# Kernel optimization log

Measured on AMD Instinct MI355X. Metric: run time of the kernel, lower is better.

## Reference

```python
import jax, jax.numpy as jnp
import numpy as np

N_NODES = 100000
N_EDGES = 800000
H_DIM = 128
E_DIM = 32
N_LAYER = 3


def setup_inputs() -> dict:
    key = jax.random.key(0)
    ks = jax.random.split(key, 5)
    x = jax.random.normal(ks[0], (N_NODES, H_DIM), dtype=jnp.float32)
    edge_index = jax.random.randint(ks[1], (2, N_EDGES), 0, N_NODES, dtype=jnp.int64)
    edge_attr = jax.random.normal(ks[2], (N_EDGES, E_DIM), dtype=jnp.float32)
    fan_in = 2 * H_DIM + E_DIM
    # torch Linear weight layout: [out_features, in_features]
    Wm = jax.random.normal(ks[3], (N_LAYER, H_DIM, fan_in), dtype=jnp.float32) / jnp.sqrt(fan_in)
    bm = jax.random.normal(ks[4], (N_LAYER, H_DIM), dtype=jnp.float32) * 0.01
    return {"x": x, "edge_index": edge_index, "edge_attr": edge_attr, "Wm": Wm, "bm": bm}


def reference(x, edge_index, edge_attr, Wm, bm):
    # PyG flow='source_to_target': row 0 = source (j), row 1 = target (i)
    src = edge_index[0]
    dst = edge_index[1]
    n_nodes = x.shape[0]
    n_layer = Wm.shape[0]
    for l in range(n_layer):  # small fixed layer count
        # message: m_ij = Linear(cat[x_j, x_i, edge_attr])
        m = jnp.concatenate([x[src], x[dst], edge_attr], axis=1)  # [E, 2h+e]
        m = jnp.einsum('ef,hf->eh', m, Wm[l]) + bm[l]             # [E, h]
        # aggr='add': scatter-add messages to target nodes
        x = jax.ops.segment_sum(m, dst, num_segments=n_nodes)     # [N, h]
        x = jax.nn.leaky_relu(x, negative_slope=0.01)
    # residual_connection='none' -> no-op; activate_last=True
    x = jax.nn.leaky_relu(x, negative_slope=0.01)
    return x
```

## Files before the change

kernel.cpp:

```cpp
#include <hip/hip_runtime.h>

#define N_NODES 100000
#define NP      100096
#define N_EDGES 800000
#define HD 128
#define ED 32
#define FAN 288
#define NL 3

#define SCHUNK 2048
#define SBLK   ((N_NODES + SCHUNK - 1) / SCHUNK)

#define TM 32

typedef short bf16x8 __attribute__((ext_vector_type(8)));
typedef short bf16x4 __attribute__((ext_vector_type(4)));
typedef float f32x4  __attribute__((ext_vector_type(4)));

__device__ inline float b2f(short s) {
    unsigned u = ((unsigned)(unsigned short)s) << 16;
    return __builtin_bit_cast(float, u);
}
__device__ inline short f2b(float f) {
    unsigned u = __builtin_bit_cast(unsigned, f);
    unsigned r = u + 0x7FFFu + ((u >> 16) & 1u);
    return (short)(r >> 16);
}


__global__ void count_kernel(const int* __restrict__ dst, int* __restrict__ deg) {
    int e = blockIdx.x * 256 + threadIdx.x;
    if (e < N_EDGES) atomicAdd(&deg[dst[e]], 1);
}

__global__ void scan_reduce(const int* __restrict__ deg, int* __restrict__ bsum) {
    __shared__ int ws[4];
    const int tid = threadIdx.x;
    int i0 = blockIdx.x * SCHUNK + tid * 8;
    int t = 0;
    #pragma unroll
    for (int j = 0; j < 8; ++j) {
        int i = i0 + j;
        if (i < N_NODES) t += deg[i];
    }
    #pragma unroll
    for (int off = 32; off >= 1; off >>= 1) t += __shfl_down(t, off, 64);
    if ((tid & 63) == 0) ws[tid >> 6] = t;
    __syncthreads();
    if (tid == 0) bsum[blockIdx.x] = ws[0] + ws[1] + ws[2] + ws[3];
}

__global__ void scan_final(const int* __restrict__ deg, const int* __restrict__ bsum,
                           int* __restrict__ ptr, int* __restrict__ cursor) {
    __shared__ int wsum[4];
    __shared__ int s_boff;
    const int tid = threadIdx.x;
    const int lane = tid & 63, wid = tid >> 6;
    if (wid == 0) {
        int v = (lane < SBLK) ? bsum[lane] : 0;
        int s = v;
        #pragma unroll
        for (int off = 1; off < 64; off <<= 1) {
            int t = __shfl_up(s, off, 64);
            if (lane >= off) s += t;
        }
        int srcl = (blockIdx.x == 0) ? 0 : (int)blockIdx.x - 1;
        int bprev = __shfl(s, srcl, 64);
        if (lane == 0) s_boff = (blockIdx.x == 0) ? 0 : bprev;
        int total = __shfl(s, SBLK - 1, 64);
        if (blockIdx.x == 0 && lane == 0) ptr[N_NODES] = total;
    }
    __syncthreads();

    int i0 = blockIdx.x * SCHUNK + tid * 8;
    int v[8]; int tsum = 0;
    #pragma unroll
    for (int j = 0; j < 8; ++j) {
        int i = i0 + j;
        v[j] = (i < N_NODES) ? deg[i] : 0;
        tsum += v[j];
    }
    int s = tsum;
    #pragma unroll
    for (int off = 1; off < 64; off <<= 1) {
        int t = __shfl_up(s, off, 64);
        if (lane >= off) s += t;
    }
    if (lane == 63) wsum[wid] = s;
    __syncthreads();
    int woff = 0;
    #pragma unroll
    for (int w = 0; w < 4; ++w) if (w < wid) woff += wsum[w];
    int excl = s_boff + woff + (s - tsum);
    #pragma unroll
    for (int j = 0; j < 8; ++j) {
        int i = i0 + j;
        if (i < N_NODES) { ptr[i] = excl; cursor[i] = excl; }
        excl += v[j];
    }
}

__global__ void fill_kernel(const int* __restrict__ src, const int* __restrict__ dst,
                            int* __restrict__ cursor, int2* __restrict__ csr2) {
    int e = blockIdx.x * 256 + threadIdx.x;
    if (e < N_EDGES) {
        int d = dst[e];
        int slot = atomicAdd(&cursor[d], 1);
        csr2[slot] = make_int2(src[e], e);
    }
}

__global__ void edge_sum(const int2* __restrict__ csr2, const int* __restrict__ ptr,
                         const float* __restrict__ eattr,
                         short* __restrict__ agge, float* __restrict__ degf) {
    int node = blockIdx.x * 32 + (threadIdx.x >> 3);
    int g = threadIdx.x & 7;
    if (node >= N_NODES) return;
    int s0 = ptr[node], s1 = ptr[node + 1];
    float4 a0 = make_float4(0.f,0.f,0.f,0.f), a1 = make_float4(0.f,0.f,0.f,0.f);
    int s = s0;
    int e0 = (s     < s1) ? csr2[s].y     : 0;
    int e1 = (s + 1 < s1) ? csr2[s + 1].y : 0;
    int e2 = (s + 2 < s1) ? csr2[s + 2].y : 0;
    int e3 = (s + 3 < s1) ? csr2[s + 3].y : 0;
    while (s + 4 <= s1) {
        float4 v0 = *reinterpret_cast<const float4*>(eattr + (size_t)e0 * ED + g * 4);
        float4 v1 = *reinterpret_cast<const float4*>(eattr + (size_t)e1 * ED + g * 4);
        float4 v2 = *reinterpret_cast<const float4*>(eattr + (size_t)e2 * ED + g * 4);
        float4 v3 = *reinterpret_cast<const float4*>(eattr + (size_t)e3 * ED + g * 4);
        s += 4;
        e0 = (s     < s1) ? csr2[s].y     : 0;
        e1 = (s + 1 < s1) ? csr2[s + 1].y : 0;
        e2 = (s + 2 < s1) ? csr2[s + 2].y : 0;
        e3 = (s + 3 < s1) ? csr2[s + 3].y : 0;
        a0.x += v0.x; a0.y += v0.y; a0.z += v0.z; a0.w += v0.w;
        a1.x += v1.x; a1.y += v1.y; a1.z += v1.z; a1.w += v1.w;
        a0.x += v2.x; a0.y += v2.y; a0.z += v2.z; a0.w += v2.w;
        a1.x += v3.x; a1.y += v3.y; a1.z += v3.z; a1.w += v3.w;
    }
    int rem = s1 - s;
    if (rem > 0) {
        float4 v = *reinterpret_cast<const float4*>(eattr + (size_t)e0 * ED + g * 4);
        a0.x += v.x; a0.y += v.y; a0.z += v.z; a0.w += v.w;
    }
    if (rem > 1) {
        float4 v = *reinterpret_cast<const float4*>(eattr + (size_t)e1 * ED + g * 4);
        a1.x += v.x; a1.y += v.y; a1.z += v.z; a1.w += v.w;
    }
    if (rem > 2) {
        float4 v = *reinterpret_cast<const float4*>(eattr + (size_t)e2 * ED + g * 4);
        a0.x += v.x; a0.y += v.y; a0.z += v.z; a0.w += v.w;
    }
    bf16x4 o;
    o[0] = f2b(a0.x + a1.x); o[1] = f2b(a0.y + a1.y);
    o[2] = f2b(a0.z + a1.z); o[3] = f2b(a0.w + a1.w);
    *reinterpret_cast<bf16x4*>(agge + (size_t)node * ED + g * 4) = o;
    if (g == 0) degf[node] = (float)(s1 - s0);
}

#define NW4 (NL * HD * FAN / 4)
#define NX4 (N_NODES * (HD / 4))
__global__ void conv_kernel(const float* __restrict__ Wm, short* __restrict__ Wb,
                            const float* __restrict__ x, short* __restrict__ xb) {
    int i4 = blockIdx.x * 256 + threadIdx.x;
    if (i4 < NW4) {
        float4 v = reinterpret_cast<const float4*>(Wm)[i4];
        bf16x4 o;
        o[0] = f2b(v.x); o[1] = f2b(v.y); o[2] = f2b(v.z); o[3] = f2b(v.w);
        reinterpret_cast<bf16x4*>(Wb)[i4] = o;
    }
    int j4 = i4 - NW4;
    if (j4 >= 0 && j4 < NX4) {
        float4 v = reinterpret_cast<const float4*>(x)[j4];
        bf16x4 o;
        o[0] = f2b(v.x); o[1] = f2b(v.y); o[2] = f2b(v.z); o[3] = f2b(v.w);
        reinterpret_cast<bf16x4*>(xb)[j4] = o;
    }
}

__global__ __launch_bounds__(256) void fused_layer(
    const int* __restrict__ ptr, const int2* __restrict__ csr2,
    const short* __restrict__ xprev,
    const short* __restrict__ agge,
    const float* __restrict__ degf,
    const short* __restrict__ Wb,
    const float* __restrict__ b,
    float* __restrict__ out_f32,
    short* __restrict__ out_x,
    int last)
{
    __shared__ char As[TM * 256];
    const int tid = threadIdx.x;
    const int m0 = blockIdx.x * TM;

    {
        const int ng = tid >> 4, g = tid & 15;
        #pragma unroll
        for (int i = 0; i < 2; ++i) {
            int row = i * 16 + ng;
            int node = m0 + row;
            float acc0[8] = {}, acc1[8] = {};
            if (node < N_NODES) {
                int s0 = ptr[node], s1 = ptr[node + 1];
                int s = s0;
                int i0 = (s     < s1) ? csr2[s].x     : 0;
                int i1 = (s + 1 < s1) ? csr2[s + 1].x : 0;
                int i2 = (s + 2 < s1) ? csr2[s + 2].x : 0;
                int i3 = (s + 3 < s1) ? csr2[s + 3].x : 0;
                while (s + 4 <= s1) {
                    bf16x8 v0 = *reinterpret_cast<const bf16x8*>(xprev + (size_t)i0 * HD + g * 8);
                    bf16x8 v1 = *reinterpret_cast<const bf16x8*>(xprev + (size_t)i1 * HD + g * 8);
                    bf16x8 v2 = *reinterpret_cast<const bf16x8*>(xprev + (size_t)i2 * HD + g * 8);
                    bf16x8 v3 = *reinterpret_cast<const bf16x8*>(xprev + (size_t)i3 * HD + g * 8);
                    s += 4;
                    i0 = (s     < s1) ? csr2[s].x     : 0;
                    i1 = (s + 1 < s1) ? csr2[s + 1].x : 0;
                    i2 = (s + 2 < s1) ? csr2[s + 2].x : 0;
                    i3 = (s + 3 < s1) ? csr2[s + 3].x : 0;
                    #pragma unroll
                    for (int j = 0; j < 8; ++j) acc0[j] += b2f(v0[j]);
                    #pragma unroll
                    for (int j = 0; j < 8; ++j) acc1[j] += b2f(v1[j]);
                    #pragma unroll
                    for (int j = 0; j < 8; ++j) acc0[j] += b2f(v2[j]);
                    #pragma unroll
                    for (int j = 0; j < 8; ++j) acc1[j] += b2f(v3[j]);
                }
                int rem = s1 - s;
                if (rem > 0) {
                    bf16x8 v = *reinterpret_cast<const bf16x8*>(xprev + (size_t)i0 * HD + g * 8);
                    #pragma unroll
                    for (int j = 0; j < 8; ++j) acc0[j] += b2f(v[j]);
                }
                if (rem > 1) {
                    bf16x8 v = *reinterpret_cast<const bf16x8*>(xprev + (size_t)i1 * HD + g * 8);
                    #pragma unroll
                    for (int j = 0; j < 8; ++j) acc1[j] += b2f(v[j]);
                }
                if (rem > 2) {
                    bf16x8 v = *reinterpret_cast<const bf16x8*>(xprev + (size_t)i2 * HD + g * 8);
                    #pragma unroll
                    for (int j = 0; j < 8; ++j) acc0[j] += b2f(v[j]);
                }
            }
            bf16x8 o;
            #pragma unroll
            for (int j = 0; j < 8; ++j) o[j] = f2b(acc0[j] + acc1[j]);
            int byte = row * 256 + g * 16;
            byte ^= (row & 7) << 4;
            *reinterpret_cast<bf16x8*>(As + byte) = o;
        }
    }
    __syncthreads();

    const int w = tid >> 6, lane = tid & 63;
    const int l15 = lane & 15, lq = lane >> 4;
    const int kb = lq * 8;

    f32x4 acc1[2][2], acc2[2][2];
    #pragma unroll
    for (int i = 0; i < 2; ++i)
        #pragma unroll
        for (int j = 0; j < 2; ++j) {
            acc1[i][j] = (f32x4){0.f, 0.f, 0.f, 0.f};
            acc2[i][j] = (f32x4){0.f, 0.f, 0.f, 0.f};
        }

    #pragma unroll
    for (int kt = 0; kt < 4; ++kt) {
        bf16x8 a[2], bf[2];
        #pragma unroll
        for (int mf = 0; mf < 2; ++mf) {
            int row = mf * 16 + l15;
            int byte = row * 256 + kt * 64 + kb * 2;
            byte ^= (row & 7) << 4;
            a[mf] = *reinterpret_cast<const bf16x8*>(As + byte);
        }
        #pragma unroll
        for (int nf = 0; nf < 2; ++nf) {
            int c = w * 32 + nf * 16 + l15;
            bf[nf] = *reinterpret_cast<const bf16x8*>(Wb + (size_t)c * FAN + kt * 32 + kb);
        }
        #pragma unroll
        for (int mf = 0; mf < 2; ++mf)
            #pragma unroll
            for (int nf = 0; nf < 2; ++nf)
                acc1[mf][nf] = __builtin_amdgcn_mfma_f32_16x16x32_bf16(
                    a[mf], bf[nf], acc1[mf][nf], 0, 0, 0);
    }
    #pragma unroll
    for (int kt = 4; kt < 9; ++kt) {
        bf16x8 a[2], bf[2];
        #pragma unroll
        for (int mf = 0; mf < 2; ++mf) {
            size_t arow = (size_t)(m0 + mf * 16 + l15);
            a[mf] = (kt < 8)
                ? *reinterpret_cast<const bf16x8*>(xprev + arow * HD + (kt * 32 - 128) + kb)
                : *reinterpret_cast<const bf16x8*>(agge + arow * ED + kb);
        }
        #pragma unroll
        for (int nf = 0; nf < 2; ++nf) {
            int c = w * 32 + nf * 16 + l15;
            bf[nf] = *reinterpret_cast<const bf16x8*>(Wb + (size_t)c * FAN + kt * 32 + kb);
        }
        #pragma unroll
        for (int mf = 0; mf < 2; ++mf)
            #pragma unroll
            for (int nf = 0; nf < 2; ++nf) {
                if (kt < 8)
                    acc2[mf][nf] = __builtin_amdgcn_mfma_f32_16x16x32_bf16(
                        a[mf], bf[nf], acc2[mf][nf], 0, 0, 0);
                else
                    acc1[mf][nf] = __builtin_amdgcn_mfma_f32_16x16x32_bf16(
                        a[mf], bf[nf], acc1[mf][nf], 0, 0, 0);
            }
    }

    #pragma unroll
    for (int mf = 0; mf < 2; ++mf) {
        int r0 = m0 + mf * 16 + lq * 4;
        float dg[4];
        #pragma unroll
        for (int j = 0; j < 4; ++j)
            dg[j] = (r0 + j < N_NODES) ? degf[r0 + j] : 0.f;
        #pragma unroll
        for (int nf = 0; nf < 2; ++nf) {
            int c = w * 32 + nf * 16 + l15;
            float bc = b[c];
            #pragma unroll
            for (int j = 0; j < 4; ++j) {
                int row = r0 + j;
                if (row >= N_NODES) continue;
                float v = acc1[mf][nf][j] + dg[j] * (acc2[mf][nf][j] + bc);
                v = (v >= 0.f) ? v : 0.01f * v;
                if (last) {
                    v = (v >= 0.f) ? v : 0.01f * v;
                    out_f32[(size_t)row * HD + c] = v;
                } else {
                    out_x[(size_t)row * HD + c] = f2b(v);
                }
            }
        }
    }
}

extern "C" void kernel_launch(void* const* d_in, const int* in_sizes, int n_in,
                              void* d_out, int out_size, void* d_ws, size_t ws_size,
                              hipStream_t stream) {
    const float* x_in  = (const float*)d_in[0];
    const int*   ei    = (const int*)d_in[1];
    const float* eattr = (const float*)d_in[2];
    const float* Wm    = (const float*)d_in[3];
    const float* bm    = (const float*)d_in[4];
    float* out = (float*)d_out;

    char* ws = (char*)d_ws;
    size_t off = 0;
    auto alloc = [&](size_t bytes) -> void* {
        void* p = ws + off;
        off = (off + bytes + 255) & ~(size_t)255;
        return p;
    };
    short* x0      = (short*)alloc((size_t)NP * HD * 2);
    short* x1      = (short*)alloc((size_t)NP * HD * 2);
    short* agge    = (short*)alloc((size_t)NP * ED * 2);
    float* degf    = (float*)alloc((size_t)NP * 4);
    int*   deg     = (int*)alloc((size_t)N_NODES * 4);
    int*   ptr     = (int*)alloc((size_t)(N_NODES + 1) * 4);
    int*   cursor  = (int*)alloc((size_t)N_NODES * 4);
    int2*  csr2    = (int2*)alloc((size_t)N_EDGES * 8);
    short* Wb      = (short*)alloc((size_t)NL * HD * FAN * 2);
    int*   bsum    = (int*)alloc((size_t)SBLK * 4);

    const int* src = ei;
    const int* dst = ei + N_EDGES;

    hipMemsetAsync(deg, 0, (size_t)N_NODES * 4, stream);
    count_kernel<<<(N_EDGES + 255) / 256, 256, 0, stream>>>(dst, deg);
    scan_reduce<<<SBLK, 256, 0, stream>>>(deg, bsum);
    scan_final<<<SBLK, 256, 0, stream>>>(deg, bsum, ptr, cursor);
    fill_kernel<<<(N_EDGES + 255) / 256, 256, 0, stream>>>(src, dst, cursor, csr2);
    edge_sum<<<(N_NODES + 31) / 32, 256, 0, stream>>>(csr2, ptr, eattr, agge, degf);
    conv_kernel<<<(NW4 + NX4 + 255) / 256, 256, 0, stream>>>(Wm, Wb, x_in, x0);

    short* xping[2] = {x0, x1};
    for (int l = 0; l < NL; ++l) {
        fused_layer<<<NP / TM, 256, 0, stream>>>(
            ptr, csr2, xping[l & 1], agge, degf,
            Wb + (size_t)l * HD * FAN, bm + (size_t)l * HD,
            out, xping[(l + 1) & 1], (l == NL - 1) ? 1 : 0);
    }
}
```

Measured before the change: 348.4 us.

## Prescale x by degree into a separate buffer and halve the row tile

Adds a second bf16 copy of node features that is pre-multiplied by in-degree. It is produced in conv_kernel and in each layer's epilogue, so the GEMM can accumulate into one set of accumulators instead of two. The fused layer also shrinks to 16 rows and 128 threads per block, with each wave covering 64 output columns. The aim is lower register pressure and higher occupancy. The cost is an extra full feature-array write per layer, more weight reloads per row, and an extra bf16 rounding of deg*x.

```diff
diff --git a/kernel.cpp b/kernel.cpp
--- a/kernel.cpp
+++ b/kernel.cpp
@@ -11,7 +11,8 @@
 #define SCHUNK 2048
 #define SBLK   ((N_NODES + SCHUNK - 1) / SCHUNK)
 
-#define TM 32
+#define TM 16
+#define THREADS 128
 
 typedef short bf16x8 __attribute__((ext_vector_type(8)));
 typedef short bf16x4 __attribute__((ext_vector_type(4)));
@@ -161,7 +162,8 @@
 #define NW4 (NL * HD * FAN / 4)
 #define NX4 (N_NODES * (HD / 4))
 __global__ void conv_kernel(const float* __restrict__ Wm, short* __restrict__ Wb,
-                            const float* __restrict__ x, short* __restrict__ xb) {
+                            const float* __restrict__ x, const float* __restrict__ degf,
+                            short* __restrict__ xb, short* __restrict__ xd) {
     int i4 = blockIdx.x * 256 + threadIdx.x;
     if (i4 < NW4) {
         float4 v = reinterpret_cast<const float4*>(Wm)[i4];
@@ -171,22 +173,33 @@
     }
     int j4 = i4 - NW4;
     if (j4 >= 0 && j4 < NX4) {
+        int row = j4 >> 5;
+        float d = degf[row];
         float4 v = reinterpret_cast<const float4*>(x)[j4];
-        bf16x4 o;
-        o[0] = f2b(v.x); o[1] = f2b(v.y); o[2] = f2b(v.z); o[3] = f2b(v.w);
+        float vv[4] = {v.x, v.y, v.z, v.w};
+        bf16x4 o, od;
+        #pragma unroll
+        for (int j = 0; j < 4; ++j) {
+            short s = f2b(vv[j]);
+            o[j] = s;
+            od[j] = f2b(b2f(s) * d);
+        }
         reinterpret_cast<bf16x4*>(xb)[j4] = o;
-    }
-}
-
-__global__ __launch_bounds__(256) void fused_layer(
+        reinterpret_cast<bf16x4*>(xd)[j4] = od;
+    }
+}
+
+__global__ __launch_bounds__(THREADS) void fused_layer(
     const int* __restrict__ ptr, const int2* __restrict__ csr2,
     const short* __restrict__ xprev,
+    const short* __restrict__ xdeg,
     const short* __restrict__ agge,
     const float* __restrict__ degf,
     const short* __restrict__ Wb,
     const float* __restrict__ b,
     float* __restrict__ out_f32,
     short* __restrict__ out_x,
+    short* __restrict__ out_xd,
     int last)
 {
     __shared__ char As[TM * 256];
@@ -197,7 +210,7 @@
         const int ng = tid >> 4, g = tid & 15;
         #pragma unroll
         for (int i = 0; i < 2; ++i) {
-            int row = i * 16 + ng;
+            int row = i * 8 + ng;
             int node = m0 + row;
             float acc0[8] = {}, acc1[8] = {};
             if (node < N_NODES) {
@@ -257,87 +270,61 @@
     const int l15 = lane & 15, lq = lane >> 4;
     const int kb = lq * 8;
 
-    f32x4 acc1[2][2], acc2[2][2];
-    #pragma unroll
-    for (int i = 0; i < 2; ++i)
-        #pragma unroll
-        for (int j = 0; j < 2; ++j) {
-            acc1[i][j] = (f32x4){0.f, 0.f, 0.f, 0.f};
-            acc2[i][j] = (f32x4){0.f, 0.f, 0.f, 0.f};
-        }
+    f32x4 acc[4];
+    #pragma unroll
+    for (int j = 0; j < 4; ++j) acc[j] = (f32x4){0.f, 0.f, 0.f, 0.f};
 
     #pragma unroll
     for (int kt = 0; kt < 4; ++kt) {
-        bf16x8 a[2], bf[2];
-        #pragma unroll
-        for (int mf = 0; mf < 2; ++mf) {
-            int row = mf * 16 + l15;
-            int byte = row * 256 + kt * 64 + kb * 2;
-            byte ^= (row & 7) << 4;
-            a[mf] = *reinterpret_cast<const bf16x8*>(As + byte);
-        }
-        #pragma unroll
-        for (int nf = 0; nf < 2; ++nf) {
-            int c = w * 32 + nf * 16 + l15;
-            bf[nf] = *reinterpret_cast<const bf16x8*>(Wb + (size_t)c * FAN + kt * 32 + kb);
-        }
-        #pragma unroll
-        for (int mf = 0; mf < 2; ++mf)
-            #pragma unroll
-            for (int nf = 0; nf < 2; ++nf)
-                acc1[mf][nf] = __builtin_amdgcn_mfma_f32_16x16x32_bf16(
-                    a[mf], bf[nf], acc1[mf][nf], 0, 0, 0);
+        int byte = l15 * 256 + kt * 64 + kb * 2;
+        byte ^= (l15 & 7) << 4;
+        bf16x8 a = *reinterpret_cast<const bf16x8*>(As + byte);
+        #pragma unroll
+        for (int nf = 0; nf < 4; ++nf) {
+            int c = w * 64 + nf * 16 + l15;
+            bf16x8 bfr = *reinterpret_cast<const bf16x8*>(Wb + (size_t)c * FAN + kt * 32 + kb);
+            acc[nf] = __builtin_amdgcn_mfma_f32_16x16x32_bf16(a, bfr, acc[nf], 0, 0, 0);
+        }
     }
     #pragma unroll
     for (int kt = 4; kt < 9; ++kt) {
-        bf16x8 a[2], bf[2];
-        #pragma unroll
-        for (int mf = 0; mf < 2; ++mf) {
-            size_t arow = (size_t)(m0 + mf * 16 + l15);
-            a[mf] = (kt < 8)
-                ? *reinterpret_cast<const bf16x8*>(xprev + arow * HD + (kt * 32 - 128) + kb)
-                : *reinterpret_cast<const bf16x8*>(agge + arow * ED + kb);
-        }
-        #pragma unroll
-        for (int nf = 0; nf < 2; ++nf) {
-            int c = w * 32 + nf * 16 + l15;
-            bf[nf] = *reinterpret_cast<const bf16x8*>(Wb + (size_t)c * FAN + kt * 32 + kb);
-        }
-        #pragma unroll
-        for (int mf = 0; mf < 2; ++mf)
-            #pragma unroll
-            for (int nf = 0; nf < 2; ++nf) {
-                if (kt < 8)
-                    acc2[mf][nf] = __builtin_amdgcn_mfma_f32_16x16x32_bf16(
-                        a[mf], bf[nf], acc2[mf][nf], 0, 0, 0);
-                else
-                    acc1[mf][nf] = __builtin_amdgcn_mfma_f32_16x16x32_bf16(
-                        a[mf], bf[nf], acc1[mf][nf], 0, 0, 0);
-            }
-    }
-
-    #pragma unroll
-    for (int mf = 0; mf < 2; ++mf) {
-        int r0 = m0 + mf * 16 + lq * 4;
+        size_t arow = (size_t)(m0 + l15);
+        bf16x8 a = (kt < 8)
+            ? *reinterpret_cast<const bf16x8*>(xdeg + arow * HD + (kt * 32 - 128) + kb)
+            : *reinterpret_cast<const bf16x8*>(agge + arow * ED + kb);
+        #pragma unroll
+        for (int nf = 0; nf < 4; ++nf) {
+            int c = w * 64 + nf * 16 + l15;
+            bf16x8 bfr = *reinterpret_cast<const bf16x8*>(Wb + (size_t)c * FAN + kt * 32 + kb);
+            acc[nf] = __builtin_amdgcn_mfma_f32_16x16x32_bf16(a, bfr, acc[nf], 0, 0, 0);
+        }
+    }
+
+    __syncthreads();
+
+    {
+        int r0 = m0 + lq * 4;
         float dg[4];
         #pragma unroll
         for (int j = 0; j < 4; ++j)
             dg[j] = (r0 + j < N_NODES) ? degf[r0 + j] : 0.f;
         #pragma unroll
-        for (int nf = 0; nf < 2; ++nf) {
-            int c = w * 32 + nf * 16 + l15;
+        for (int nf = 0; nf < 4; ++nf) {
+            int c = w * 64 + nf * 16 + l15;
             float bc = b[c];
             #pragma unroll
             for (int j = 0; j < 4; ++j) {
                 int row = r0 + j;
                 if (row >= N_NODES) continue;
-                float v = acc1[mf][nf][j] + dg[j] * (acc2[mf][nf][j] + bc);
+                float v = acc[nf][j] + dg[j] * bc;
                 v = (v >= 0.f) ? v : 0.01f * v;
                 if (last) {
                     v = (v >= 0.f) ? v : 0.01f * v;
                     out_f32[(size_t)row * HD + c] = v;
                 } else {
-                    out_x[(size_t)row * HD + c] = f2b(v);
+                    short xb = f2b(v);
+                    out_x[(size_t)row * HD + c] = xb;
+                    out_xd[(size_t)row * HD + c] = f2b(b2f(xb) * dg[j]);
                 }
             }
         }
@@ -363,6 +350,7 @@
     };
     short* x0      = (short*)alloc((size_t)NP * HD * 2);
     short* x1      = (short*)alloc((size_t)NP * HD * 2);
+    short* xdeg    = (short*)alloc((size_t)NP * HD * 2);
     short* agge    = (short*)alloc((size_t)NP * ED * 2);
     float* degf    = (float*)alloc((size_t)NP * 4);
     int*   deg     = (int*)alloc((size_t)N_NODES * 4);
@@ -381,13 +369,13 @@
     scan_final<<<SBLK, 256, 0, stream>>>(deg, bsum, ptr, cursor);
     fill_kernel<<<(N_EDGES + 255) / 256, 256, 0, stream>>>(src, dst, cursor, csr2);
     edge_sum<<<(N_NODES + 31) / 32, 256, 0, stream>>>(csr2, ptr, eattr, agge, degf);
-    conv_kernel<<<(NW4 + NX4 + 255) / 256, 256, 0, stream>>>(Wm, Wb, x_in, x0);
+    conv_kernel<<<(NW4 + NX4 + 255) / 256, 256, 0, stream>>>(Wm, Wb, x_in, degf, x0, xdeg);
 
     short* xping[2] = {x0, x1};
     for (int l = 0; l < NL; ++l) {
-        fused_layer<<<NP / TM, 256, 0, stream>>>(
-            ptr, csr2, xping[l & 1], agge, degf,
+        fused_layer<<<NP / TM, THREADS, 0, stream>>>(
+            ptr, csr2, xping[l & 1], xdeg, agge, degf,
             Wb + (size_t)l * HD * FAN, bm + (size_t)l * HD,
-            out, xping[(l + 1) & 1], (l == NL - 1) ? 1 : 0);
-    }
-}
+            out, xping[(l + 1) & 1], xdeg, (l == NL - 1) ? 1 : 0);
+    }
+}
```

After: 353.3 us. Within noise of the previous version (+1.4%).

## Split CSR into SoA arrays with int4 index loads and prescale x by degree

Applied to the files above, without the earlier changes.

The interleaved int2 CSR is split into separate source-index and edge-id arrays. The gather loops in edge_sum and fused_layer now read indices four at a time as aligned int4 vectors, with masking at the segment edges. A degree-scaled bf16 copy of x (xdeg) is also kept and updated each layer. The self-term GEMM then uses it directly, which merges the two MFMA accumulators into one and simplifies the epilogue. In exchange, each layer writes an extra bf16 node-feature array, rounding changes slightly because x·deg is rounded to bf16 before the matmul, and xdeg is updated in place.

```diff
diff --git a/kernel.cpp b/kernel.cpp
--- a/kernel.cpp
+++ b/kernel.cpp
@@ -101,16 +101,18 @@
 }
 
 __global__ void fill_kernel(const int* __restrict__ src, const int* __restrict__ dst,
-                            int* __restrict__ cursor, int2* __restrict__ csr2) {
+                            int* __restrict__ cursor,
+                            int* __restrict__ csr_src, int* __restrict__ csr_eid) {
     int e = blockIdx.x * 256 + threadIdx.x;
     if (e < N_EDGES) {
         int d = dst[e];
         int slot = atomicAdd(&cursor[d], 1);
-        csr2[slot] = make_int2(src[e], e);
-    }
-}
-
-__global__ void edge_sum(const int2* __restrict__ csr2, const int* __restrict__ ptr,
+        csr_src[slot] = src[e];
+        csr_eid[slot] = e;
+    }
+}
+
+__global__ void edge_sum(const int* __restrict__ csr_eid, const int* __restrict__ ptr,
                          const float* __restrict__ eattr,
                          short* __restrict__ agge, float* __restrict__ degf) {
     int node = blockIdx.x * 32 + (threadIdx.x >> 3);
@@ -118,38 +120,41 @@
     if (node >= N_NODES) return;
     int s0 = ptr[node], s1 = ptr[node + 1];
     float4 a0 = make_float4(0.f,0.f,0.f,0.f), a1 = make_float4(0.f,0.f,0.f,0.f);
-    int s = s0;
-    int e0 = (s     < s1) ? csr2[s].y     : 0;
-    int e1 = (s + 1 < s1) ? csr2[s + 1].y : 0;
-    int e2 = (s + 2 < s1) ? csr2[s + 2].y : 0;
-    int e3 = (s + 3 < s1) ? csr2[s + 3].y : 0;
-    while (s + 4 <= s1) {
-        float4 v0 = *reinterpret_cast<const float4*>(eattr + (size_t)e0 * ED + g * 4);
-        float4 v1 = *reinterpret_cast<const float4*>(eattr + (size_t)e1 * ED + g * 4);
-        float4 v2 = *reinterpret_cast<const float4*>(eattr + (size_t)e2 * ED + g * 4);
-        float4 v3 = *reinterpret_cast<const float4*>(eattr + (size_t)e3 * ED + g * 4);
-        s += 4;
-        e0 = (s     < s1) ? csr2[s].y     : 0;
-        e1 = (s + 1 < s1) ? csr2[s + 1].y : 0;
-        e2 = (s + 2 < s1) ? csr2[s + 2].y : 0;
-        e3 = (s + 3 < s1) ? csr2[s + 3].y : 0;
-        a0.x += v0.x; a0.y += v0.y; a0.z += v0.z; a0.w += v0.w;
-        a1.x += v1.x; a1.y += v1.y; a1.z += v1.z; a1.w += v1.w;
-        a0.x += v2.x; a0.y += v2.y; a0.z += v2.z; a0.w += v2.w;
-        a1.x += v3.x; a1.y += v3.y; a1.z += v3.z; a1.w += v3.w;
-    }
-    int rem = s1 - s;
-    if (rem > 0) {
-        float4 v = *reinterpret_cast<const float4*>(eattr + (size_t)e0 * ED + g * 4);
-        a0.x += v.x; a0.y += v.y; a0.z += v.z; a0.w += v.w;
-    }
-    if (rem > 1) {
-        float4 v = *reinterpret_cast<const float4*>(eattr + (size_t)e1 * ED + g * 4);
-        a1.x += v.x; a1.y += v.y; a1.z += v.z; a1.w += v.w;
-    }
-    if (rem > 2) {
-        float4 v = *reinterpret_cast<const float4*>(eattr + (size_t)e2 * ED + g * 4);
-        a0.x += v.x; a0.y += v.y; a0.z += v.z; a0.w += v.w;
+    int b0 = s0 >> 2;
+    int nb = ((s1 + 3) >> 2) - b0;
+    const int4* ep = (const int4*)csr_eid + b0;
+    int4 cur = (nb > 0) ? ep[0] : make_int4(0,0,0,0);
+    for (int t = 0; t < nb; ++t) {
+        int4 nxt = (t + 1 < nb) ? ep[t + 1] : make_int4(0,0,0,0);
+        int base = (b0 + t) * 4;
+        if (base >= s0 && base + 4 <= s1) {
+            float4 v0 = *reinterpret_cast<const float4*>(eattr + (size_t)cur.x * ED + g * 4);
+            float4 v1 = *reinterpret_cast<const float4*>(eattr + (size_t)cur.y * ED + g * 4);
+            float4 v2 = *reinterpret_cast<const float4*>(eattr + (size_t)cur.z * ED + g * 4);
+            float4 v3 = *reinterpret_cast<const float4*>(eattr + (size_t)cur.w * ED + g * 4);
+            a0.x += v0.x; a0.y += v0.y; a0.z += v0.z; a0.w += v0.w;
+            a1.x += v1.x; a1.y += v1.y; a1.z += v1.z; a1.w += v1.w;
+            a0.x += v2.x; a0.y += v2.y; a0.z += v2.z; a0.w += v2.w;
+            a1.x += v3.x; a1.y += v3.y; a1.z += v3.z; a1.w += v3.w;
+        } else {
+            if (base + 0 >= s0 && base + 0 < s1) {
+                float4 v = *reinterpret_cast<const float4*>(eattr + (size_t)cur.x * ED + g * 4);
+                a0.x += v.x; a0.y += v.y; a0.z += v.z; a0.w += v.w;
+            }
+            if (base + 1 >= s0 && base + 1 < s1) {
+                float4 v = *reinterpret_cast<const float4*>(eattr + (size_t)cur.y * ED + g * 4);
+                a1.x += v.x; a1.y += v.y; a1.z += v.z; a1.w += v.w;
+            }
+            if (base + 2 >= s0 && base + 2 < s1) {
+                float4 v = *reinterpret_cast<const float4*>(eattr + (size_t)cur.z * ED + g * 4);
+                a0.x += v.x; a0.y += v.y; a0.z += v.z; a0.w += v.w;
+            }
+            if (base + 3 >= s0 && base + 3 < s1) {
+                float4 v = *reinterpret_cast<const float4*>(eattr + (size_t)cur.w * ED + g * 4);
+                a1.x += v.x; a1.y += v.y; a1.z += v.z; a1.w += v.w;
+            }
+        }
+        cur = nxt;
     }
     bf16x4 o;
     o[0] = f2b(a0.x + a1.x); o[1] = f2b(a0.y + a1.y);
@@ -161,7 +166,8 @@
 #define NW4 (NL * HD * FAN / 4)
 #define NX4 (N_NODES * (HD / 4))
 __global__ void conv_kernel(const float* __restrict__ Wm, short* __restrict__ Wb,
-                            const float* __restrict__ x, short* __restrict__ xb) {
+                            const float* __restrict__ x, const float* __restrict__ degf,
+                            short* __restrict__ xb, short* __restrict__ xd) {
     int i4 = blockIdx.x * 256 + threadIdx.x;
     if (i4 < NW4) {
         float4 v = reinterpret_cast<const float4*>(Wm)[i4];
@@ -171,22 +177,33 @@
     }
     int j4 = i4 - NW4;
     if (j4 >= 0 && j4 < NX4) {
+        int row = j4 >> 5;
+        float d = degf[row];
         float4 v = reinterpret_cast<const float4*>(x)[j4];
-        bf16x4 o;
-        o[0] = f2b(v.x); o[1] = f2b(v.y); o[2] = f2b(v.z); o[3] = f2b(v.w);
+        float vv[4] = {v.x, v.y, v.z, v.w};
+        bf16x4 o, od;
+        #pragma unroll
+        for (int j = 0; j < 4; ++j) {
+            short s = f2b(vv[j]);
+            o[j] = s;
+            od[j] = f2b(b2f(s) * d);
+        }
         reinterpret_cast<bf16x4*>(xb)[j4] = o;
+        reinterpret_cast<bf16x4*>(xd)[j4] = od;
     }
 }
 
 __global__ __launch_bounds__(256) void fused_layer(
-    const int* __restrict__ ptr, const int2* __restrict__ csr2,
+    const int* __restrict__ ptr, const int* __restrict__ csr_src,
     const short* __restrict__ xprev,
+    const short* __restrict__ xdeg,
     const short* __restrict__ agge,
     const float* __restrict__ degf,
     const short* __restrict__ Wb,
     const float* __restrict__ b,
     float* __restrict__ out_f32,
     short* __restrict__ out_x,
+    short* __restrict__ out_xd,
     int last)
 {
     __shared__ char As[TM * 256];
@@ -202,45 +219,49 @@
             float acc0[8] = {}, acc1[8] = {};
             if (node < N_NODES) {
                 int s0 = ptr[node], s1 = ptr[node + 1];
-                int s = s0;
-                int i0 = (s     < s1) ? csr2[s].x     : 0;
-                int i1 = (s + 1 < s1) ? csr2[s + 1].x : 0;
-                int i2 = (s + 2 < s1) ? csr2[s + 2].x : 0;
-                int i3 = (s + 3 < s1) ? csr2[s + 3].x : 0;
-                while (s + 4 <= s1) {
-                    bf16x8 v0 = *reinterpret_cast<const bf16x8*>(xprev + (size_t)i0 * HD + g * 8);
-                    bf16x8 v1 = *reinterpret_cast<const bf16x8*>(xprev + (size_t)i1 * HD + g * 8);
-                    bf16x8 v2 = *reinterpret_cast<const bf16x8*>(xprev + (size_t)i2 * HD + g * 8);
-                    bf16x8 v3 = *reinterpret_cast<const bf16x8*>(xprev + (size_t)i3 * HD + g * 8);
-                    s += 4;
-                    i0 = (s     < s1) ? csr2[s].x     : 0;
-                    i1 = (s + 1 < s1) ? csr2[s + 1].x : 0;
-                    i2 = (s + 2 < s1) ? csr2[s + 2].x : 0;
-                    i3 = (s + 3 < s1) ? csr2[s + 3].x : 0;
-                    #pragma unroll
-                    for (int j = 0; j < 8; ++j) acc0[j] += b2f(v0[j]);
-                    #pragma unroll
-                    for (int j = 0; j < 8; ++j) acc1[j] += b2f(v1[j]);
-                    #pragma unroll
-                    for (int j = 0; j < 8; ++j) acc0[j] += b2f(v2[j]);
-                    #pragma unroll
-                    for (int j = 0; j < 8; ++j) acc1[j] += b2f(v3[j]);
-                }
-                int rem = s1 - s;
-                if (rem > 0) {
-                    bf16x8 v = *reinterpret_cast<const bf16x8*>(xprev + (size_t)i0 * HD + g * 8);
-                    #pragma unroll
-                    for (int j = 0; j < 8; ++j) acc0[j] += b2f(v[j]);
-                }
-                if (rem > 1) {
-                    bf16x8 v = *reinterpret_cast<const bf16x8*>(xprev + (size_t)i1 * HD + g * 8);
-                    #pragma unroll
-                    for (int j = 0; j < 8; ++j) acc1[j] += b2f(v[j]);
-                }
-                if (rem > 2) {
-                    bf16x8 v = *reinterpret_cast<const bf16x8*>(xprev + (size_t)i2 * HD + g * 8);
-                    #pragma unroll
-                    for (int j = 0; j < 8; ++j) acc0[j] += b2f(v[j]);
+                int b0 = s0 >> 2;
+                int nb = ((s1 + 3) >> 2) - b0;
+                const int4* sp = (const int4*)csr_src + b0;
+                int4 cur = (nb > 0) ? sp[0] : make_int4(0,0,0,0);
+                for (int t = 0; t < nb; ++t) {
+                    int4 nxt = (t + 1 < nb) ? sp[t + 1] : make_int4(0,0,0,0);
+                    int base = (b0 + t) * 4;
+                    if (base >= s0 && base + 4 <= s1) {
+                        bf16x8 v0 = *reinterpret_cast<const bf16x8*>(xprev + (size_t)cur.x * HD + g * 8);
+                        bf16x8 v1 = *reinterpret_cast<const bf16x8*>(xprev + (size_t)cur.y * HD + g * 8);
+                        bf16x8 v2 = *reinterpret_cast<const bf16x8*>(xprev + (size_t)cur.z * HD + g * 8);
+                        bf16x8 v3 = *reinterpret_cast<const bf16x8*>(xprev + (size_t)cur.w * HD + g * 8);
+                        #pragma unroll
+                        for (int j = 0; j < 8; ++j) acc0[j] += b2f(v0[j]);
+                        #pragma unroll
+                        for (int j = 0; j < 8; ++j) acc1[j] += b2f(v1[j]);
+                        #pragma unroll
+                        for (int j = 0; j < 8; ++j) acc0[j] += b2f(v2[j]);
+                        #pragma unroll
+                        for (int j = 0; j < 8; ++j) acc1[j] += b2f(v3[j]);
+                    } else {
+                        if (base + 0 >= s0 && base + 0 < s1) {
+                            bf16x8 v = *reinterpret_cast<const bf16x8*>(xprev + (size_t)cur.x * HD + g * 8);
+                            #pragma unroll
+                            for (int j = 0; j < 8; ++j) acc0[j] += b2f(v[j]);
+                        }
+                        if (base + 1 >= s0 && base + 1 < s1) {
+                            bf16x8 v = *reinterpret_cast<const bf16x8*>(xprev + (size_t)cur.y * HD + g * 8);
+                            #pragma unroll
+                            for (int j = 0; j < 8; ++j) acc1[j] += b2f(v[j]);
+                        }
+                        if (base + 2 >= s0 && base + 2 < s1) {
+                            bf16x8 v = *reinterpret_cast<const bf16x8*>(xprev + (size_t)cur.z * HD + g * 8);
+                            #pragma unroll
+                            for (int j = 0; j < 8; ++j) acc0[j] += b2f(v[j]);
+                        }
+                        if (base + 3 >= s0 && base + 3 < s1) {
+                            bf16x8 v = *reinterpret_cast<const bf16x8*>(xprev + (size_t)cur.w * HD + g * 8);
+                            #pragma unroll
+                            for (int j = 0; j < 8; ++j) acc1[j] += b2f(v[j]);
+                        }
+                    }
+                    cur = nxt;
                 }
             }
             bf16x8 o;
@@ -257,14 +278,11 @@
     const int l15 = lane & 15, lq = lane >> 4;
     const int kb = lq * 8;
 
-    f32x4 acc1[2][2], acc2[2][2];
+    f32x4 acc[2][2];
     #pragma unroll
     for (int i = 0; i < 2; ++i)
         #pragma unroll
-        for (int j = 0; j < 2; ++j) {
-            acc1[i][j] = (f32x4){0.f, 0.f, 0.f, 0.f};
-            acc2[i][j] = (f32x4){0.f, 0.f, 0.f, 0.f};
-        }
+        for (int j = 0; j < 2; ++j) acc[i][j] = (f32x4){0.f, 0.f, 0.f, 0.f};
 
     #pragma unroll
     for (int kt = 0; kt < 4; ++kt) {
@@ -285,8 +303,8 @@
         for (int mf = 0; mf < 2; ++mf)
             #pragma unroll
             for (int nf = 0; nf < 2; ++nf)
-                acc1[mf][nf] = __builtin_amdgcn_mfma_f32_16x16x32_bf16(
-                    a[mf], bf[nf], acc1[mf][nf], 0, 0, 0);
+                acc[mf][nf] = __builtin_amdgcn_mfma_f32_16x16x32_bf16(
+                    a[mf], bf[nf], acc[mf][nf], 0, 0, 0);
     }
     #pragma unroll
     for (int kt = 4; kt < 9; ++kt) {
@@ -295,7 +313,7 @@
         for (int mf = 0; mf < 2; ++mf) {
             size_t arow = (size_t)(m0 + mf * 16 + l15);
             a[mf] = (kt < 8)
-                ? *reinterpret_cast<const bf16x8*>(xprev + arow * HD + (kt * 32 - 128) + kb)
+                ? *reinterpret_cast<const bf16x8*>(xdeg + arow * HD + (kt * 32 - 128) + kb)
                 : *reinterpret_cast<const bf16x8*>(agge + arow * ED + kb);
         }
         #pragma unroll
@@ -306,15 +324,12 @@
         #pragma unroll
         for (int mf = 0; mf < 2; ++mf)
             #pragma unroll
-            for (int nf = 0; nf < 2; ++nf) {
-                if (kt < 8)
-                    acc2[mf][nf] = __builtin_amdgcn_mfma_f32_16x16x32_bf16(
-                        a[mf], bf[nf], acc2[mf][nf], 0, 0, 0);
-                else
-                    acc1[mf][nf] = __builtin_amdgcn_mfma_f32_16x16x32_bf16(
-                        a[mf], bf[nf], acc1[mf][nf], 0, 0, 0);
-            }
-    }
+            for (int nf = 0; nf < 2; ++nf)
+                acc[mf][nf] = __builtin_amdgcn_mfma_f32_16x16x32_bf16(
+                    a[mf], bf[nf], acc[mf][nf], 0, 0, 0);
+    }
+
+    __syncthreads();
 
     #pragma unroll
     for (int mf = 0; mf < 2; ++mf) {
@@ -331,13 +346,15 @@
             for (int j = 0; j < 4; ++j) {
                 int row = r0 + j;
                 if (row >= N_NODES) continue;
-                float v = acc1[mf][nf][j] + dg[j] * (acc2[mf][nf][j] + bc);
+                float v = acc[mf][nf][j] + dg[j] * bc;
                 v = (v >= 0.f) ? v : 0.01f * v;
                 if (last) {
                     v = (v >= 0.f) ? v : 0.01f * v;
                     out_f32[(size_t)row * HD + c] = v;
                 } else {
-                    out_x[(size_t)row * HD + c] = f2b(v);
+                    short xb = f2b(v);
+                    out_x[(size_t)row * HD + c] = xb;
+                    out_xd[(size_t)row * HD + c] = f2b(b2f(xb) * dg[j]);
                 }
             }
         }
@@ -363,12 +380,14 @@
     };
     short* x0      = (short*)alloc((size_t)NP * HD * 2);
     short* x1      = (short*)alloc((size_t)NP * HD * 2);
+    short* xdeg    = (short*)alloc((size_t)NP * HD * 2);
     short* agge    = (short*)alloc((size_t)NP * ED * 2);
     float* degf    = (float*)alloc((size_t)NP * 4);
     int*   deg     = (int*)alloc((size_t)N_NODES * 4);
     int*   ptr     = (int*)alloc((size_t)(N_NODES + 1) * 4);
     int*   cursor  = (int*)alloc((size_t)N_NODES * 4);
-    int2*  csr2    = (int2*)alloc((size_t)N_EDGES * 8);
+    int*   csr_src = (int*)alloc((size_t)(N_EDGES + 8) * 4);
+    int*   csr_eid = (int*)alloc((size_t)(N_EDGES + 8) * 4);
     short* Wb      = (short*)alloc((size_t)NL * HD * FAN * 2);
     int*   bsum    = (int*)alloc((size_t)SBLK * 4);
 
@@ -379,15 +398,15 @@
     count_kernel<<<(N_EDGES + 255) / 256, 256, 0, stream>>>(dst, deg);
     scan_reduce<<<SBLK, 256, 0, stream>>>(deg, bsum);
     scan_final<<<SBLK, 256, 0, stream>>>(deg, bsum, ptr, cursor);
-    fill_kernel<<<(N_EDGES + 255) / 256, 256, 0, stream>>>(src, dst, cursor, csr2);
-    edge_sum<<<(N_NODES + 31) / 32, 256, 0, stream>>>(csr2, ptr, eattr, agge, degf);
-    conv_kernel<<<(NW4 + NX4 + 255) / 256, 256, 0, stream>>>(Wm, Wb, x_in, x0);
+    fill_kernel<<<(N_EDGES + 255) / 256, 256, 0, stream>>>(src, dst, cursor, csr_src, csr_eid);
+    edge_sum<<<(N_NODES + 31) / 32, 256, 0, stream>>>(csr_eid, ptr, eattr, agge, degf);
+    conv_kernel<<<(NW4 + NX4 + 255) / 256, 256, 0, stream>>>(Wm, Wb, x_in, degf, x0, xdeg);
 
     short* xping[2] = {x0, x1};
     for (int l = 0; l < NL; ++l) {
         fused_layer<<<NP / TM, 256, 0, stream>>>(
-            ptr, csr2, xping[l & 1], agge, degf,
+            ptr, csr_src, xping[l & 1], xdeg, agge, degf,
             Wb + (size_t)l * HD * FAN, bm + (size_t)l * HD,
-            out, xping[(l + 1) & 1], (l == NL - 1) ? 1 : 0);
-    }
-}
+            out, xping[(l + 1) & 1], xdeg, (l == NL - 1) ? 1 : 0);
+    }
+}
```

Measured after the change: 413.3 us. 18.6% more time.
